# Performance work log

Measured on AMD Instinct MI355X. Metric: run time of the kernel, lower is better.

## Reference

```python
import jax, jax.numpy as jnp
import numpy as np

B, C, L = 256, 500, 200
D, H, NUM_ITEMS = 64, 128, 100000
BETA = 0.7
EPS = 1e-8


def _xavier(key, fan_in, fan_out):
    lim = float(np.sqrt(6.0 / (fan_in + fan_out)))
    return jax.random.uniform(key, (fan_in, fan_out), minval=-lim, maxval=lim, dtype=jnp.float32)


def setup_inputs() -> dict:
    key = jax.random.key(0)
    ks = jax.random.split(key, 12)
    inp = {
        'candidate_items': jax.random.randint(ks[0], (B, C), 0, NUM_ITEMS, dtype=jnp.int64) if jax.config.read('jax_enable_x64') else jax.random.randint(ks[0], (B, C), 0, NUM_ITEMS),
        'query_times': jax.random.uniform(ks[1], (B,), dtype=jnp.float32),
        'candidate_histories': jax.random.uniform(ks[2], (B, C, L), dtype=jnp.float32),
        'item_emb': 0.02 * jax.random.normal(ks[3], (NUM_ITEMS, D), dtype=jnp.float32),
        'base_W1': _xavier(ks[4], D, H), 'base_b1': jnp.zeros((H,), jnp.float32),
        'base_W2': _xavier(ks[5], H, H), 'base_b2': jnp.zeros((H,), jnp.float32),
        'base_W3': _xavier(ks[6], H, 1),
        'exc_W1': _xavier(ks[7], D, H), 'exc_b1': jnp.zeros((H,), jnp.float32),
        'exc_W2': _xavier(ks[8], H, H), 'exc_b2': jnp.zeros((H,), jnp.float32),
        'exc_W3': _xavier(ks[9], H, 1),
    }
    return inp


def _mlp(x, W1, b1, W2, b2, W3):
    # (Linear + Softplus) x depth, then Linear -> 1 (no bias), squeeze last dim
    h = jax.nn.softplus(x @ W1 + b1)
    h = jax.nn.softplus(h @ W2 + b2)
    return (h @ W3)[..., 0]


def reference(candidate_items, query_times, candidate_histories, item_emb,
              base_W1, base_b1, base_W2, base_b2, base_W3,
              exc_W1, exc_b1, exc_W2, exc_b2, exc_W3):
    z = item_emb[candidate_items]                                  # [B, C, D]
    mu = jax.nn.softplus(_mlp(z, base_W1, base_b1, base_W2, base_b2, base_W3)) + EPS   # [B, C]
    alpha = jax.nn.softplus(_mlp(z, exc_W1, exc_b1, exc_W2, exc_b2, exc_W3)) + EPS     # [B, C]
    q = query_times[:, None, None]                                 # [B, 1, 1]
    mask = candidate_histories < q                                 # [B, C, L]
    delta = jnp.maximum(q - candidate_histories, 0.0)              # clamp(min=0)
    h = jnp.sum(jnp.exp(-BETA * delta) * mask, axis=-1)            # [B, C]
    return mu + alpha * h
```

## Files before the change

### kernel.cpp

```cpp
#include <hip/hip_runtime.h>
#include <math.h>

#define BB 256
#define CC 500
#define LL 200
#define DD 64
#define HH 128
#define NUM_ITEMS 100000
#define BETA 0.7f
#define EPSV 1e-8f

#define TM 32
#define WPB 4
#define NTILE (NUM_ITEMS / TM)
#define BPS 1024

typedef _Float16 half8 __attribute__((ext_vector_type(8)));
typedef float floatx4 __attribute__((ext_vector_type(4)));

__device__ __forceinline__ float softplus_safe(float x) {
    float t = __expf(-fabsf(x));
    return fmaxf(x, 0.0f) + __logf(1.0f + t);
}
__device__ __forceinline__ float softplus_fast(float x) {
    return __logf(1.0f + __expf(x));
}
__device__ __forceinline__ float softplus_small(float x) {
    float z = x * x;
    float p = fmaf(fmaf(-5.2083333e-3f, z, 0.125f), z, 0.69314718f);
    return fmaf(x, 0.5f, p);
}

__global__ __launch_bounds__(256) void prep_w(
    const float* __restrict__ W1, const float* __restrict__ W2,
    const float* __restrict__ V1, const float* __restrict__ V2,
    _Float16* __restrict__ wb)
{
    int t = blockIdx.x * 256 + threadIdx.x;
    if (t >= 49152) return;
    float v;
    if (t < 8192)       { int n = t >> 6,  k = t & 63;             v = W1[k * HH + n]; }
    else if (t < 24576) { int u = t - 8192;  int n = u >> 7, k = u & 127; v = W2[k * HH + n]; }
    else if (t < 32768) { int u = t - 24576; int n = u >> 6, k = u & 63;  v = V1[k * HH + n]; }
    else                { int u = t - 32768; int n = u >> 7, k = u & 127; v = V2[k * HH + n]; }
    wb[t] = (_Float16)v;
}

__global__ __launch_bounds__(256, 4) void mlp_mfma(
    const float* __restrict__ emb, const _Float16* __restrict__ wb,
    const float* __restrict__ b1, const float* __restrict__ b2, const float* __restrict__ W3,
    const float* __restrict__ c1, const float* __restrict__ c2, const float* __restrict__ V3,
    float* __restrict__ mu, float* __restrict__ alpha)
{
    __shared__ __align__(16) _Float16 h1s[TM * HH];
    __shared__ __align__(16) float    part[TM * WPB];
    int tid  = threadIdx.x;
    int w    = tid >> 6, lane = tid & 63;
    int quad = lane >> 4, l15 = lane & 15;

    int is_exc = blockIdx.x >= BPS;
    int bslot  = blockIdx.x - (is_exc ? BPS : 0);

    const _Float16* W1t = wb + (is_exc ? 24576 : 0);
    const _Float16* W2t = wb + (is_exc ? 32768 : 8192);
    const float* B1  = is_exc ? c1 : b1;
    const float* B2  = is_exc ? c2 : b2;
    const float* W3p = is_exc ? V3 : W3;
    float* outp = is_exc ? alpha : mu;

    half8 w1f[2][2];
    half8 w2f[4][2];
    float b1v[2], b2v[2], w3v[2];
    #pragma unroll
    for (int n = 0; n < 2; ++n) {
        int j = (2 * w + n) * 16 + l15;
        b1v[n] = B1[j];
        b2v[n] = B2[j];
        w3v[n] = W3p[j];
        #pragma unroll
        for (int kt = 0; kt < 2; ++kt)
            w1f[kt][n] = *(const half8*)(W1t + j * DD + kt * 32 + quad * 8);
        #pragma unroll
        for (int kt = 0; kt < 4; ++kt)
            w2f[kt][n] = *(const half8*)(W2t + j * HH + kt * 32 + quad * 8);
    }

    #pragma unroll 1
    for (int t = bslot; t < NTILE; t += BPS) {
        half8 zf[2][2];
        #pragma unroll
        for (int mt = 0; mt < 2; ++mt) {
            const float* p = emb + (size_t)(t * TM + mt * 16 + l15) * DD + quad * 8;
            #pragma unroll
            for (int kt = 0; kt < 2; ++kt) {
                floatx4 v0 = *(const floatx4*)(p + kt * 32);
                floatx4 v1 = *(const floatx4*)(p + kt * 32 + 4);
                half8 z;
                #pragma unroll
                for (int j = 0; j < 4; ++j) {
                    z[j] = (_Float16)v0[j]; z[4 + j] = (_Float16)v1[j];
                }
                zf[mt][kt] = z;
            }
        }

        floatx4 acc1[2][2];
        #pragma unroll
        for (int n = 0; n < 2; ++n) {
            float bv = b1v[n];
            #pragma unroll
            for (int mt = 0; mt < 2; ++mt) acc1[mt][n] = (floatx4){bv, bv, bv, bv};
        }
        #pragma unroll
        for (int kt = 0; kt < 2; ++kt)
            #pragma unroll
            for (int n = 0; n < 2; ++n)
                #pragma unroll
                for (int mt = 0; mt < 2; ++mt)
                    acc1[mt][n] = __builtin_amdgcn_mfma_f32_16x16x32_f16(zf[mt][kt], w1f[kt][n], acc1[mt][n], 0, 0, 0);
        #pragma unroll
        for (int mt = 0; mt < 2; ++mt)
            #pragma unroll
            for (int n = 0; n < 2; ++n)
                #pragma unroll
                for (int r = 0; r < 4; ++r) {
                    int itq = quad * 4 + r;
                    int sw  = ((2 * w + n) * 2 + (l15 >> 3)) ^ itq;
                    h1s[(mt * 16 + itq) * HH + sw * 8 + (l15 & 7)] =
                        (_Float16)softplus_small(acc1[mt][n][r]);
                }
        __syncthreads();

        floatx4 acc2[2][2];
        #pragma unroll
        for (int n = 0; n < 2; ++n) {
            float bv = b2v[n];
            #pragma unroll
            for (int mt = 0; mt < 2; ++mt) acc2[mt][n] = (floatx4){bv, bv, bv, bv};
        }
        #pragma unroll
        for (int kt = 0; kt < 4; ++kt) {
            half8 af[2];
            #pragma unroll
            for (int mt = 0; mt < 2; ++mt)
                af[mt] = *(const half8*)(h1s + (mt * 16 + l15) * HH + (((kt * 4 + quad) ^ l15) * 8));
            #pragma unroll
            for (int n = 0; n < 2; ++n)
                #pragma unroll
                for (int mt = 0; mt < 2; ++mt)
                    acc2[mt][n] = __builtin_amdgcn_mfma_f32_16x16x32_f16(af[mt], w2f[kt][n], acc2[mt][n], 0, 0, 0);
        }
        float sacc[2][4];
        #pragma unroll
        for (int mt = 0; mt < 2; ++mt)
            #pragma unroll
            for (int r = 0; r < 4; ++r) sacc[mt][r] = 0.0f;
        #pragma unroll
        for (int n = 0; n < 2; ++n) {
            float w3 = w3v[n];
            #pragma unroll
            for (int mt = 0; mt < 2; ++mt)
                #pragma unroll
                for (int r = 0; r < 4; ++r)
                    sacc[mt][r] += softplus_fast(acc2[mt][n][r]) * w3;
        }
        #pragma unroll
        for (int mt = 0; mt < 2; ++mt)
            #pragma unroll
            for (int r = 0; r < 4; ++r) {
                float s = sacc[mt][r];
                s += __shfl_xor(s, 1, 64);
                s += __shfl_xor(s, 2, 64);
                s += __shfl_xor(s, 4, 64);
                s += __shfl_xor(s, 8, 64);
                if (l15 == 0)
                    part[(mt * 16 + quad * 4 + r) * WPB + w] = s;
            }
        __syncthreads();

        if (tid < TM) {
            floatx4 pv = *(const floatx4*)(part + tid * WPB);
            float s = (pv[0] + pv[1]) + (pv[2] + pv[3]);
            outp[t * TM + tid] = softplus_safe(s) + EPSV;
        }
    }
}

__global__ __launch_bounds__(256) void hawkes_kernel(
    const int* __restrict__ items,
    const float* __restrict__ qt,
    const float* __restrict__ hist,
    const float* __restrict__ mu,
    const float* __restrict__ alpha,
    float* __restrict__ out)
{
    int w = blockIdx.x * 4 + (threadIdx.x >> 6);
    int lane = threadIdx.x & 63;
    float q = qt[w / CC];

    float s = 0.0f;
    if (lane < LL / 4) {
        float4 v = *(const float4*)(hist + (size_t)w * LL + lane * 4);
        s  = (v.x < q) ? __expf(BETA * v.x) : 0.f;
        s += (v.y < q) ? __expf(BETA * v.y) : 0.f;
        s += (v.z < q) ? __expf(BETA * v.z) : 0.f;
        s += (v.w < q) ? __expf(BETA * v.w) : 0.f;
    }
    #pragma unroll
    for (int off = 1; off < 64; off <<= 1) s += __shfl_xor(s, off, 64);

    if (lane == 0) {
        int it = items[w];
        out[w] = fmaf(alpha[it] * __expf(-BETA * q), s, mu[it]);
    }
}

extern "C" void kernel_launch(void* const* d_in, const int* in_sizes, int n_in,
                              void* d_out, int out_size, void* d_ws, size_t ws_size,
                              hipStream_t stream)
{
    const int*   items = (const int*)  d_in[0];
    const float* qt    = (const float*)d_in[1];
    const float* hist  = (const float*)d_in[2];
    const float* emb   = (const float*)d_in[3];
    const float* W1    = (const float*)d_in[4];
    const float* b1    = (const float*)d_in[5];
    const float* W2    = (const float*)d_in[6];
    const float* b2    = (const float*)d_in[7];
    const float* W3    = (const float*)d_in[8];
    const float* V1    = (const float*)d_in[9];
    const float* c1    = (const float*)d_in[10];
    const float* V2    = (const float*)d_in[11];
    const float* c2    = (const float*)d_in[12];
    const float* V3    = (const float*)d_in[13];

    float* out = (float*)d_out;
    _Float16* wb = (_Float16*)d_ws;
    float* mu    = (float*)((char*)d_ws + 98304);
    float* alpha = mu + NUM_ITEMS;

    prep_w<<<192, 256, 0, stream>>>(W1, W2, V1, V2, wb);

    mlp_mfma<<<2 * BPS, WPB * 64, 0, stream>>>(emb, wb, b1, b2, W3, c1, c2, V3, mu, alpha);

    hawkes_kernel<<<(BB * CC) / 4, 256, 0, stream>>>(items, qt, hist, mu, alpha, out);
}
```

Measured before the change: 239.9 us.

## Interleave MLP tiles with history-reduction blocks in one fused launch

```diff
diff --git a/kernel.cpp b/kernel.cpp
--- a/kernel.cpp
+++ b/kernel.cpp
@@ -11,9 +11,11 @@
 #define EPSV 1e-8f
 
 #define TM 32
-#define WPB 4
 #define NTILE (NUM_ITEMS / TM)
-#define BPS 1024
+#define NMLPID (2 * NTILE)
+#define HROWS (BB * CC)
+#define HBLK (HROWS / 4)
+#define GRID 38400
 
 typedef _Float16 half8 __attribute__((ext_vector_type(8)));
 typedef float floatx4 __attribute__((ext_vector_type(4)));
@@ -46,20 +48,45 @@
     wb[t] = (_Float16)v;
 }
 
-__global__ __launch_bounds__(256, 4) void mlp_mfma(
+__global__ __launch_bounds__(256, 4) void fused(
     const float* __restrict__ emb, const _Float16* __restrict__ wb,
     const float* __restrict__ b1, const float* __restrict__ b2, const float* __restrict__ W3,
     const float* __restrict__ c1, const float* __restrict__ c2, const float* __restrict__ V3,
-    float* __restrict__ mu, float* __restrict__ alpha)
+    float* __restrict__ mu, float* __restrict__ alpha,
+    const float* __restrict__ qt, const float* __restrict__ hist,
+    float* __restrict__ hsum)
 {
     __shared__ __align__(16) _Float16 h1s[TM * HH];
-    __shared__ __align__(16) float    part[TM * WPB];
+    __shared__ __align__(16) float    part[TM * 4];
     int tid  = threadIdx.x;
+    int bx   = blockIdx.x;
+
+    if (bx % 6 != 0) {
+        int hid  = bx - bx / 6 - 1;
+        int lane = tid & 63;
+        int row  = hid * 4 + (tid >> 6);
+        float q  = qt[row / CC];
+        float s = 0.0f;
+        if (lane < LL / 4) {
+            float4 v = *(const float4*)(hist + (size_t)row * LL + lane * 4);
+            s  = (v.x < q) ? __expf(BETA * v.x) : 0.f;
+            s += (v.y < q) ? __expf(BETA * v.y) : 0.f;
+            s += (v.z < q) ? __expf(BETA * v.z) : 0.f;
+            s += (v.w < q) ? __expf(BETA * v.w) : 0.f;
+        }
+        #pragma unroll
+        for (int off = 1; off < 64; off <<= 1) s += __shfl_xor(s, off, 64);
+        if (lane == 0) hsum[row] = s;
+        return;
+    }
+
+    int mid = bx / 6;
+    if (mid >= NMLPID) return;
+    int is_exc = mid >= NTILE;
+    int t      = mid - (is_exc ? NTILE : 0);
+
     int w    = tid >> 6, lane = tid & 63;
     int quad = lane >> 4, l15 = lane & 15;
-
-    int is_exc = blockIdx.x >= BPS;
-    int bslot  = blockIdx.x - (is_exc ? BPS : 0);
 
     const _Float16* W1t = wb + (is_exc ? 24576 : 0);
     const _Float16* W2t = wb + (is_exc ? 32768 : 8192);
@@ -85,134 +112,114 @@
             w2f[kt][n] = *(const half8*)(W2t + j * HH + kt * 32 + quad * 8);
     }
 
-    #pragma unroll 1
-    for (int t = bslot; t < NTILE; t += BPS) {
-        half8 zf[2][2];
-        #pragma unroll
-        for (int mt = 0; mt < 2; ++mt) {
-            const float* p = emb + (size_t)(t * TM + mt * 16 + l15) * DD + quad * 8;
-            #pragma unroll
-            for (int kt = 0; kt < 2; ++kt) {
-                floatx4 v0 = *(const floatx4*)(p + kt * 32);
-                floatx4 v1 = *(const floatx4*)(p + kt * 32 + 4);
-                half8 z;
-                #pragma unroll
-                for (int j = 0; j < 4; ++j) {
-                    z[j] = (_Float16)v0[j]; z[4 + j] = (_Float16)v1[j];
-                }
-                zf[mt][kt] = z;
+    half8 zf[2][2];
+    #pragma unroll
+    for (int mt = 0; mt < 2; ++mt) {
+        const float* p = emb + (size_t)(t * TM + mt * 16 + l15) * DD + quad * 8;
+        #pragma unroll
+        for (int kt = 0; kt < 2; ++kt) {
+            floatx4 v0 = *(const floatx4*)(p + kt * 32);
+            floatx4 v1 = *(const floatx4*)(p + kt * 32 + 4);
+            half8 z;
+            #pragma unroll
+            for (int j = 0; j < 4; ++j) { z[j] = (_Float16)v0[j]; z[4 + j] = (_Float16)v1[j]; }
+            zf[mt][kt] = z;
+        }
+    }
+
+    floatx4 acc1[2][2];
+    #pragma unroll
+    for (int n = 0; n < 2; ++n) {
+        float bv = b1v[n];
+        #pragma unroll
+        for (int mt = 0; mt < 2; ++mt) acc1[mt][n] = (floatx4){bv, bv, bv, bv};
+    }
+    #pragma unroll
+    for (int kt = 0; kt < 2; ++kt)
+        #pragma unroll
+        for (int n = 0; n < 2; ++n)
+            #pragma unroll
+            for (int mt = 0; mt < 2; ++mt)
+                acc1[mt][n] = __builtin_amdgcn_mfma_f32_16x16x32_f16(zf[mt][kt], w1f[kt][n], acc1[mt][n], 0, 0, 0);
+    #pragma unroll
+    for (int mt = 0; mt < 2; ++mt)
+        #pragma unroll
+        for (int n = 0; n < 2; ++n)
+            #pragma unroll
+            for (int r = 0; r < 4; ++r) {
+                int itq = quad * 4 + r;
+                int sw  = ((2 * w + n) * 2 + (l15 >> 3)) ^ itq;
+                h1s[(mt * 16 + itq) * HH + sw * 8 + (l15 & 7)] =
+                    (_Float16)softplus_small(acc1[mt][n][r]);
             }
+    __syncthreads();
+
+    floatx4 acc2[2][2];
+    #pragma unroll
+    for (int n = 0; n < 2; ++n) {
+        float bv = b2v[n];
+        #pragma unroll
+        for (int mt = 0; mt < 2; ++mt) acc2[mt][n] = (floatx4){bv, bv, bv, bv};
+    }
+    #pragma unroll
+    for (int kt = 0; kt < 4; ++kt) {
+        half8 af[2];
+        #pragma unroll
+        for (int mt = 0; mt < 2; ++mt)
+            af[mt] = *(const half8*)(h1s + (mt * 16 + l15) * HH + (((kt * 4 + quad) ^ l15) * 8));
+        #pragma unroll
+        for (int n = 0; n < 2; ++n)
+            #pragma unroll
+            for (int mt = 0; mt < 2; ++mt)
+                acc2[mt][n] = __builtin_amdgcn_mfma_f32_16x16x32_f16(af[mt], w2f[kt][n], acc2[mt][n], 0, 0, 0);
+    }
+    float sacc[2][4];
+    #pragma unroll
+    for (int mt = 0; mt < 2; ++mt)
+        #pragma unroll
+        for (int r = 0; r < 4; ++r) sacc[mt][r] = 0.0f;
+    #pragma unroll
+    for (int n = 0; n < 2; ++n) {
+        float w3 = w3v[n];
+        #pragma unroll
+        for (int mt = 0; mt < 2; ++mt)
+            #pragma unroll
+            for (int r = 0; r < 4; ++r)
+                sacc[mt][r] += softplus_fast(acc2[mt][n][r]) * w3;
+    }
+    #pragma unroll
+    for (int mt = 0; mt < 2; ++mt)
+        #pragma unroll
+        for (int r = 0; r < 4; ++r) {
+            float s = sacc[mt][r];
+            s += __shfl_xor(s, 1, 64);
+            s += __shfl_xor(s, 2, 64);
+            s += __shfl_xor(s, 4, 64);
+            s += __shfl_xor(s, 8, 64);
+            if (l15 == 0)
+                part[(mt * 16 + quad * 4 + r) * 4 + w] = s;
         }
-
-        floatx4 acc1[2][2];
-        #pragma unroll
-        for (int n = 0; n < 2; ++n) {
-            float bv = b1v[n];
-            #pragma unroll
-            for (int mt = 0; mt < 2; ++mt) acc1[mt][n] = (floatx4){bv, bv, bv, bv};
-        }
-        #pragma unroll
-        for (int kt = 0; kt < 2; ++kt)
-            #pragma unroll
-            for (int n = 0; n < 2; ++n)
-                #pragma unroll
-                for (int mt = 0; mt < 2; ++mt)
-                    acc1[mt][n] = __builtin_amdgcn_mfma_f32_16x16x32_f16(zf[mt][kt], w1f[kt][n], acc1[mt][n], 0, 0, 0);
-        #pragma unroll
-        for (int mt = 0; mt < 2; ++mt)
-            #pragma unroll
-            for (int n = 0; n < 2; ++n)
-                #pragma unroll
-                for (int r = 0; r < 4; ++r) {
-                    int itq = quad * 4 + r;
-                    int sw  = ((2 * w + n) * 2 + (l15 >> 3)) ^ itq;
-                    h1s[(mt * 16 + itq) * HH + sw * 8 + (l15 & 7)] =
-                        (_Float16)softplus_small(acc1[mt][n][r]);
-                }
-        __syncthreads();
-
-        floatx4 acc2[2][2];
-        #pragma unroll
-        for (int n = 0; n < 2; ++n) {
-            float bv = b2v[n];
-            #pragma unroll
-            for (int mt = 0; mt < 2; ++mt) acc2[mt][n] = (floatx4){bv, bv, bv, bv};
-        }
-        #pragma unroll
-        for (int kt = 0; kt < 4; ++kt) {
-            half8 af[2];
-            #pragma unroll
-            for (int mt = 0; mt < 2; ++mt)
-                af[mt] = *(const half8*)(h1s + (mt * 16 + l15) * HH + (((kt * 4 + quad) ^ l15) * 8));
-            #pragma unroll
-            for (int n = 0; n < 2; ++n)
-                #pragma unroll
-                for (int mt = 0; mt < 2; ++mt)
-                    acc2[mt][n] = __builtin_amdgcn_mfma_f32_16x16x32_f16(af[mt], w2f[kt][n], acc2[mt][n], 0, 0, 0);
-        }
-        float sacc[2][4];
-        #pragma unroll
-        for (int mt = 0; mt < 2; ++mt)
-            #pragma unroll
-            for (int r = 0; r < 4; ++r) sacc[mt][r] = 0.0f;
-        #pragma unroll
-        for (int n = 0; n < 2; ++n) {
-            float w3 = w3v[n];
-            #pragma unroll
-            for (int mt = 0; mt < 2; ++mt)
-                #pragma unroll
-                for (int r = 0; r < 4; ++r)
-                    sacc[mt][r] += softplus_fast(acc2[mt][n][r]) * w3;
-        }
-        #pragma unroll
-        for (int mt = 0; mt < 2; ++mt)
-            #pragma unroll
-            for (int r = 0; r < 4; ++r) {
-                float s = sacc[mt][r];
-                s += __shfl_xor(s, 1, 64);
-                s += __shfl_xor(s, 2, 64);
-                s += __shfl_xor(s, 4, 64);
-                s += __shfl_xor(s, 8, 64);
-                if (l15 == 0)
-                    part[(mt * 16 + quad * 4 + r) * WPB + w] = s;
-            }
-        __syncthreads();
-
-        if (tid < TM) {
-            floatx4 pv = *(const floatx4*)(part + tid * WPB);
-            float s = (pv[0] + pv[1]) + (pv[2] + pv[3]);
-            outp[t * TM + tid] = softplus_safe(s) + EPSV;
-        }
-    }
-}
-
-__global__ __launch_bounds__(256) void hawkes_kernel(
+    __syncthreads();
+
+    if (tid < TM) {
+        floatx4 pv = *(const floatx4*)(part + tid * 4);
+        float s = (pv[0] + pv[1]) + (pv[2] + pv[3]);
+        outp[t * TM + tid] = softplus_safe(s) + EPSV;
+    }
+}
+
+__global__ __launch_bounds__(256) void gather_kernel(
     const int* __restrict__ items,
     const float* __restrict__ qt,
-    const float* __restrict__ hist,
+    const float* __restrict__ hsum,
     const float* __restrict__ mu,
     const float* __restrict__ alpha,
     float* __restrict__ out)
 {
-    int w = blockIdx.x * 4 + (threadIdx.x >> 6);
-    int lane = threadIdx.x & 63;
-    float q = qt[w / CC];
-
-    float s = 0.0f;
-    if (lane < LL / 4) {
-        float4 v = *(const float4*)(hist + (size_t)w * LL + lane * 4);
-        s  = (v.x < q) ? __expf(BETA * v.x) : 0.f;
-        s += (v.y < q) ? __expf(BETA * v.y) : 0.f;
-        s += (v.z < q) ? __expf(BETA * v.z) : 0.f;
-        s += (v.w < q) ? __expf(BETA * v.w) : 0.f;
-    }
-    #pragma unroll
-    for (int off = 1; off < 64; off <<= 1) s += __shfl_xor(s, off, 64);
-
-    if (lane == 0) {
-        int it = items[w];
-        out[w] = fmaf(alpha[it] * __expf(-BETA * q), s, mu[it]);
-    }
+    int row = blockIdx.x * 256 + threadIdx.x;
+    float q = qt[row / CC];
+    int it = items[row];
+    out[row] = fmaf(alpha[it] * __expf(-BETA * q), hsum[row], mu[it]);
 }
 
 extern "C" void kernel_launch(void* const* d_in, const int* in_sizes, int n_in,
@@ -238,10 +245,12 @@
     _Float16* wb = (_Float16*)d_ws;
     float* mu    = (float*)((char*)d_ws + 98304);
     float* alpha = mu + NUM_ITEMS;
+    float* hsum  = alpha + NUM_ITEMS;
 
     prep_w<<<192, 256, 0, stream>>>(W1, W2, V1, V2, wb);
 
-    mlp_mfma<<<2 * BPS, WPB * 64, 0, stream>>>(emb, wb, b1, b2, W3, c1, c2, V3, mu, alpha);
-
-    hawkes_kernel<<<(BB * CC) / 4, 256, 0, stream>>>(items, qt, hist, mu, alpha, out);
-}
+    fused<<<GRID, 256, 0, stream>>>(emb, wb, b1, b2, W3, c1, c2, V3,
+                                    mu, alpha, qt, hist, hsum);
+
+    gather_kernel<<<HROWS / 256, 256, 0, stream>>>(items, qt, hsum, mu, alpha, out);
+}
```

New measurement: 283.9 us. +18.3%, slower.

## Launch one MLP tile per block and process four rows per wave in hawkes

Applied to the files above, without the earlier changes.

```diff
diff --git a/kernel.cpp b/kernel.cpp
--- a/kernel.cpp
+++ b/kernel.cpp
@@ -11,9 +11,8 @@
 #define EPSV 1e-8f
 
 #define TM 32
-#define WPB 4
 #define NTILE (NUM_ITEMS / TM)
-#define BPS 1024
+#define HROWS (BB * CC)
 
 typedef _Float16 half8 __attribute__((ext_vector_type(8)));
 typedef float floatx4 __attribute__((ext_vector_type(4)));
@@ -53,13 +52,13 @@
     float* __restrict__ mu, float* __restrict__ alpha)
 {
     __shared__ __align__(16) _Float16 h1s[TM * HH];
-    __shared__ __align__(16) float    part[TM * WPB];
+    __shared__ __align__(16) float    part[TM * 4];
     int tid  = threadIdx.x;
     int w    = tid >> 6, lane = tid & 63;
     int quad = lane >> 4, l15 = lane & 15;
 
-    int is_exc = blockIdx.x >= BPS;
-    int bslot  = blockIdx.x - (is_exc ? BPS : 0);
+    int is_exc = blockIdx.x >= NTILE;
+    int t      = blockIdx.x - (is_exc ? NTILE : 0);
 
     const _Float16* W1t = wb + (is_exc ? 24576 : 0);
     const _Float16* W2t = wb + (is_exc ? 32768 : 8192);
@@ -85,108 +84,103 @@
             w2f[kt][n] = *(const half8*)(W2t + j * HH + kt * 32 + quad * 8);
     }
 
-    #pragma unroll 1
-    for (int t = bslot; t < NTILE; t += BPS) {
-        half8 zf[2][2];
-        #pragma unroll
-        for (int mt = 0; mt < 2; ++mt) {
-            const float* p = emb + (size_t)(t * TM + mt * 16 + l15) * DD + quad * 8;
-            #pragma unroll
-            for (int kt = 0; kt < 2; ++kt) {
-                floatx4 v0 = *(const floatx4*)(p + kt * 32);
-                floatx4 v1 = *(const floatx4*)(p + kt * 32 + 4);
-                half8 z;
-                #pragma unroll
-                for (int j = 0; j < 4; ++j) {
-                    z[j] = (_Float16)v0[j]; z[4 + j] = (_Float16)v1[j];
-                }
-                zf[mt][kt] = z;
+    half8 zf[2][2];
+    #pragma unroll
+    for (int mt = 0; mt < 2; ++mt) {
+        const float* p = emb + (size_t)(t * TM + mt * 16 + l15) * DD + quad * 8;
+        #pragma unroll
+        for (int kt = 0; kt < 2; ++kt) {
+            floatx4 v0 = *(const floatx4*)(p + kt * 32);
+            floatx4 v1 = *(const floatx4*)(p + kt * 32 + 4);
+            half8 z;
+            #pragma unroll
+            for (int j = 0; j < 4; ++j) { z[j] = (_Float16)v0[j]; z[4 + j] = (_Float16)v1[j]; }
+            zf[mt][kt] = z;
+        }
+    }
+
+    floatx4 acc1[2][2];
+    #pragma unroll
+    for (int n = 0; n < 2; ++n) {
+        float bv = b1v[n];
+        #pragma unroll
+        for (int mt = 0; mt < 2; ++mt) acc1[mt][n] = (floatx4){bv, bv, bv, bv};
+    }
+    #pragma unroll
+    for (int kt = 0; kt < 2; ++kt)
+        #pragma unroll
+        for (int n = 0; n < 2; ++n)
+            #pragma unroll
+            for (int mt = 0; mt < 2; ++mt)
+                acc1[mt][n] = __builtin_amdgcn_mfma_f32_16x16x32_f16(zf[mt][kt], w1f[kt][n], acc1[mt][n], 0, 0, 0);
+    #pragma unroll
+    for (int mt = 0; mt < 2; ++mt)
+        #pragma unroll
+        for (int n = 0; n < 2; ++n)
+            #pragma unroll
+            for (int r = 0; r < 4; ++r) {
+                int itq = quad * 4 + r;
+                int sw  = ((2 * w + n) * 2 + (l15 >> 3)) ^ itq;
+                h1s[(mt * 16 + itq) * HH + sw * 8 + (l15 & 7)] =
+                    (_Float16)softplus_small(acc1[mt][n][r]);
             }
+    __syncthreads();
+
+    floatx4 acc2[2][2];
+    #pragma unroll
+    for (int n = 0; n < 2; ++n) {
+        float bv = b2v[n];
+        #pragma unroll
+        for (int mt = 0; mt < 2; ++mt) acc2[mt][n] = (floatx4){bv, bv, bv, bv};
+    }
+    #pragma unroll
+    for (int kt = 0; kt < 4; ++kt) {
+        half8 af[2];
+        #pragma unroll
+        for (int mt = 0; mt < 2; ++mt)
+            af[mt] = *(const half8*)(h1s + (mt * 16 + l15) * HH + (((kt * 4 + quad) ^ l15) * 8));
+        #pragma unroll
+        for (int n = 0; n < 2; ++n)
+            #pragma unroll
+            for (int mt = 0; mt < 2; ++mt)
+                acc2[mt][n] = __builtin_amdgcn_mfma_f32_16x16x32_f16(af[mt], w2f[kt][n], acc2[mt][n], 0, 0, 0);
+    }
+    float sacc[2][4];
+    #pragma unroll
+    for (int mt = 0; mt < 2; ++mt)
+        #pragma unroll
+        for (int r = 0; r < 4; ++r) sacc[mt][r] = 0.0f;
+    #pragma unroll
+    for (int n = 0; n < 2; ++n) {
+        float w3 = w3v[n];
+        #pragma unroll
+        for (int mt = 0; mt < 2; ++mt)
+            #pragma unroll
+            for (int r = 0; r < 4; ++r)
+                sacc[mt][r] += softplus_fast(acc2[mt][n][r]) * w3;
+    }
+    #pragma unroll
+    for (int mt = 0; mt < 2; ++mt)
+        #pragma unroll
+        for (int r = 0; r < 4; ++r) {
+            float s = sacc[mt][r];
+            s += __shfl_xor(s, 1, 64);
+            s += __shfl_xor(s, 2, 64);
+            s += __shfl_xor(s, 4, 64);
+            s += __shfl_xor(s, 8, 64);
+            if (l15 == 0)
+                part[(mt * 16 + quad * 4 + r) * 4 + w] = s;
         }
-
-        floatx4 acc1[2][2];
-        #pragma unroll
-        for (int n = 0; n < 2; ++n) {
-            float bv = b1v[n];
-            #pragma unroll
-            for (int mt = 0; mt < 2; ++mt) acc1[mt][n] = (floatx4){bv, bv, bv, bv};
-        }
-        #pragma unroll
-        for (int kt = 0; kt < 2; ++kt)
-            #pragma unroll
-            for (int n = 0; n < 2; ++n)
-                #pragma unroll
-                for (int mt = 0; mt < 2; ++mt)
-                    acc1[mt][n] = __builtin_amdgcn_mfma_f32_16x16x32_f16(zf[mt][kt], w1f[kt][n], acc1[mt][n], 0, 0, 0);
-        #pragma unroll
-        for (int mt = 0; mt < 2; ++mt)
-            #pragma unroll
-            for (int n = 0; n < 2; ++n)
-                #pragma unroll
-                for (int r = 0; r < 4; ++r) {
-                    int itq = quad * 4 + r;
-                    int sw  = ((2 * w + n) * 2 + (l15 >> 3)) ^ itq;
-                    h1s[(mt * 16 + itq) * HH + sw * 8 + (l15 & 7)] =
-                        (_Float16)softplus_small(acc1[mt][n][r]);
-                }
-        __syncthreads();
-
-        floatx4 acc2[2][2];
-        #pragma unroll
-        for (int n = 0; n < 2; ++n) {
-            float bv = b2v[n];
-            #pragma unroll
-            for (int mt = 0; mt < 2; ++mt) acc2[mt][n] = (floatx4){bv, bv, bv, bv};
-        }
-        #pragma unroll
-        for (int kt = 0; kt < 4; ++kt) {
-            half8 af[2];
-            #pragma unroll
-            for (int mt = 0; mt < 2; ++mt)
-                af[mt] = *(const half8*)(h1s + (mt * 16 + l15) * HH + (((kt * 4 + quad) ^ l15) * 8));
-            #pragma unroll
-            for (int n = 0; n < 2; ++n)
-                #pragma unroll
-                for (int mt = 0; mt < 2; ++mt)
-                    acc2[mt][n] = __builtin_amdgcn_mfma_f32_16x16x32_f16(af[mt], w2f[kt][n], acc2[mt][n], 0, 0, 0);
-        }
-        float sacc[2][4];
-        #pragma unroll
-        for (int mt = 0; mt < 2; ++mt)
-            #pragma unroll
-            for (int r = 0; r < 4; ++r) sacc[mt][r] = 0.0f;
-        #pragma unroll
-        for (int n = 0; n < 2; ++n) {
-            float w3 = w3v[n];
-            #pragma unroll
-            for (int mt = 0; mt < 2; ++mt)
-                #pragma unroll
-                for (int r = 0; r < 4; ++r)
-                    sacc[mt][r] += softplus_fast(acc2[mt][n][r]) * w3;
-        }
-        #pragma unroll
-        for (int mt = 0; mt < 2; ++mt)
-            #pragma unroll
-            for (int r = 0; r < 4; ++r) {
-                float s = sacc[mt][r];
-                s += __shfl_xor(s, 1, 64);
-                s += __shfl_xor(s, 2, 64);
-                s += __shfl_xor(s, 4, 64);
-                s += __shfl_xor(s, 8, 64);
-                if (l15 == 0)
-                    part[(mt * 16 + quad * 4 + r) * WPB + w] = s;
-            }
-        __syncthreads();
-
-        if (tid < TM) {
-            floatx4 pv = *(const floatx4*)(part + tid * WPB);
-            float s = (pv[0] + pv[1]) + (pv[2] + pv[3]);
-            outp[t * TM + tid] = softplus_safe(s) + EPSV;
-        }
-    }
-}
-
-__global__ __launch_bounds__(256) void hawkes_kernel(
+    __syncthreads();
+
+    if (tid < TM) {
+        floatx4 pv = *(const floatx4*)(part + tid * 4);
+        float s = (pv[0] + pv[1]) + (pv[2] + pv[3]);
+        outp[t * TM + tid] = softplus_safe(s) + EPSV;
+    }
+}
+
+__global__ __launch_bounds__(256) void hawkes4(
     const int* __restrict__ items,
     const float* __restrict__ qt,
     const float* __restrict__ hist,
@@ -194,24 +188,54 @@
     const float* __restrict__ alpha,
     float* __restrict__ out)
 {
-    int w = blockIdx.x * 4 + (threadIdx.x >> 6);
+    int wv   = blockIdx.x * 4 + (threadIdx.x >> 6);
     int lane = threadIdx.x & 63;
-    float q = qt[w / CC];
-
-    float s = 0.0f;
+    int row0 = wv * 4;
+
+    float q0 = qt[(row0 + 0) / CC];
+    float q1 = qt[(row0 + 1) / CC];
+    float q2 = qt[(row0 + 2) / CC];
+    float q3 = qt[(row0 + 3) / CC];
+
+    float s0 = 0.f, s1 = 0.f, s2 = 0.f, s3 = 0.f;
     if (lane < LL / 4) {
-        float4 v = *(const float4*)(hist + (size_t)w * LL + lane * 4);
-        s  = (v.x < q) ? __expf(BETA * v.x) : 0.f;
-        s += (v.y < q) ? __expf(BETA * v.y) : 0.f;
-        s += (v.z < q) ? __expf(BETA * v.z) : 0.f;
-        s += (v.w < q) ? __expf(BETA * v.w) : 0.f;
-    }
-    #pragma unroll
-    for (int off = 1; off < 64; off <<= 1) s += __shfl_xor(s, off, 64);
+        const float* base = hist + (size_t)row0 * LL + lane * 4;
+        float4 v0 = *(const float4*)(base);
+        float4 v1 = *(const float4*)(base + LL);
+        float4 v2 = *(const float4*)(base + 2 * LL);
+        float4 v3 = *(const float4*)(base + 3 * LL);
+        s0  = (v0.x < q0) ? __expf(BETA * v0.x) : 0.f;
+        s0 += (v0.y < q0) ? __expf(BETA * v0.y) : 0.f;
+        s0 += (v0.z < q0) ? __expf(BETA * v0.z) : 0.f;
+        s0 += (v0.w < q0) ? __expf(BETA * v0.w) : 0.f;
+        s1  = (v1.x < q1) ? __expf(BETA * v1.x) : 0.f;
+        s1 += (v1.y < q1) ? __expf(BETA * v1.y) : 0.f;
+        s1 += (v1.z < q1) ? __expf(BETA * v1.z) : 0.f;
+        s1 += (v1.w < q1) ? __expf(BETA * v1.w) : 0.f;
+        s2  = (v2.x < q2) ? __expf(BETA * v2.x) : 0.f;
+        s2 += (v2.y < q2) ? __expf(BETA * v2.y) : 0.f;
+        s2 += (v2.z < q2) ? __expf(BETA * v2.z) : 0.f;
+        s2 += (v2.w < q2) ? __expf(BETA * v2.w) : 0.f;
+        s3  = (v3.x < q3) ? __expf(BETA * v3.x) : 0.f;
+        s3 += (v3.y < q3) ? __expf(BETA * v3.y) : 0.f;
+        s3 += (v3.z < q3) ? __expf(BETA * v3.z) : 0.f;
+        s3 += (v3.w < q3) ? __expf(BETA * v3.w) : 0.f;
+    }
+    #pragma unroll
+    for (int off = 1; off < 64; off <<= 1) {
+        s0 += __shfl_xor(s0, off, 64);
+        s1 += __shfl_xor(s1, off, 64);
+        s2 += __shfl_xor(s2, off, 64);
+        s3 += __shfl_xor(s3, off, 64);
+    }
 
     if (lane == 0) {
-        int it = items[w];
-        out[w] = fmaf(alpha[it] * __expf(-BETA * q), s, mu[it]);
+        int i0 = items[row0], i1 = items[row0 + 1];
+        int i2 = items[row0 + 2], i3 = items[row0 + 3];
+        out[row0]     = fmaf(alpha[i0] * __expf(-BETA * q0), s0, mu[i0]);
+        out[row0 + 1] = fmaf(alpha[i1] * __expf(-BETA * q1), s1, mu[i1]);
+        out[row0 + 2] = fmaf(alpha[i2] * __expf(-BETA * q2), s2, mu[i2]);
+        out[row0 + 3] = fmaf(alpha[i3] * __expf(-BETA * q3), s3, mu[i3]);
     }
 }
 
@@ -241,7 +265,7 @@
 
     prep_w<<<192, 256, 0, stream>>>(W1, W2, V1, V2, wb);
 
-    mlp_mfma<<<2 * BPS, WPB * 64, 0, stream>>>(emb, wb, b1, b2, W3, c1, c2, V3, mu, alpha);
-
-    hawkes_kernel<<<(BB * CC) / 4, 256, 0, stream>>>(items, qt, hist, mu, alpha, out);
-}
+    mlp_mfma<<<2 * NTILE, 256, 0, stream>>>(emb, wb, b1, b2, W3, c1, c2, V3, mu, alpha);
+
+    hawkes4<<<HROWS / 16, 256, 0, stream>>>(items, qt, hist, mu, alpha, out);
+}
```

After: 244.6 us. Within noise of the previous version (+1.9%).
